# Performance work log

Hardware: AMD Instinct MI355X
Metric: run time of the kernel (lower is better)

Reference implementation:

```python
import jax, jax.numpy as jnp
import numpy as np

B, C, N, E, F = 8, 4, 2048, 512, 2048
EPS = 1e-5
MASK_SCALE = 5.0


def layer_norm(x, gamma, beta):
    mu = jnp.mean(x, axis=-1, keepdims=True)
    var = jnp.mean(jnp.square(x - mu), axis=-1, keepdims=True)
    return (x - mu) * jax.lax.rsqrt(var + EPS) * gamma + beta


def setup_inputs() -> dict:
    key = jax.random.key(0)
    ks = jax.random.split(key, 8)
    src = jax.random.normal(ks[0], (B, C, N, E), dtype=jnp.float32)
    key_padding_mask = jax.random.uniform(ks[1], (B, N), dtype=jnp.float32)
    # FFN params (torch Linear default init scale ~ U(-1/sqrt(fan_in), +))
    W1 = jax.random.normal(ks[2], (E, F), dtype=jnp.float32) / np.sqrt(E)
    b1 = jnp.zeros((F,), dtype=jnp.float32)
    W2 = jax.random.normal(ks[3], (F, E), dtype=jnp.float32) / np.sqrt(F)
    b2 = jnp.zeros((E,), dtype=jnp.float32)
    g1 = jnp.ones((E,), dtype=jnp.float32)
    be1 = jnp.zeros((E,), dtype=jnp.float32)
    g2 = jnp.ones((E,), dtype=jnp.float32)
    be2 = jnp.zeros((E,), dtype=jnp.float32)
    return {"src": src, "key_padding_mask": key_padding_mask,
            "W1": W1, "b1": b1, "W2": W2, "b2": b2,
            "g1": g1, "be1": be1, "g2": g2, "be2": be2}


def reference(src, key_padding_mask, W1, b1, W2, b2, g1, be1, g2, be2):
    # src: [B, C, N, E]; channels batched into one fused attention call
    scale = 1.0 / jnp.sqrt(jnp.asarray(src.shape[-1], src.dtype))
    scores = jnp.einsum('bcne,bcme->bcnm', src, src) * scale  # [B,C,N,N]
    scores = scores - key_padding_mask[:, None, None, :] * MASK_SCALE
    attn = jax.nn.softmax(scores, axis=-1)
    attn_out = jnp.einsum('bcnm,bcme->bcne', attn, src)
    # residual + norm1 (dropout is identity at eval)
    src2 = layer_norm(src + attn_out, g1, be1)
    # feedforward: Linear -> ReLU -> Linear
    ff = jax.nn.relu(jnp.einsum('bcne,ef->bcnf', src2, W1) + b1)
    ff = jnp.einsum('bcnf,fe->bcne', ff, W2) + b2
    out = layer_norm(src2 + ff, g2, be2)
    return out
```

## Files before the change

### kernel.cpp

```cpp
#include <hip/hip_runtime.h>
#include <stdint.h>

constexpr int CB = 8, CC = 4, CN = 2048, CE = 512, CF = 2048;
constexpr long long TOT = (long long)CB * CC * CN * CE;
constexpr int GRP = 16;
constexpr int MCH = 65536;
constexpr float SCALE = 0.04419417382415922f;
constexpr float MASK_SCALE = 5.0f;
constexpr float EPS = 1e-5f;

typedef unsigned short bf16_t;
typedef __attribute__((ext_vector_type(4))) float f32x4;
typedef __attribute__((ext_vector_type(8))) short s16x8;

#define DEV static __device__ __forceinline__

DEV unsigned short f2bf(float f) {
    unsigned u = __float_as_uint(f);
    unsigned r = (u + 0x7fffu + ((u >> 16) & 1u)) >> 16;
    return (unsigned short)r;
}
DEV float bf2f(unsigned short b) {
    return __uint_as_float(((unsigned)b) << 16);
}

typedef const __attribute__((address_space(1))) unsigned int* gptr_t;
typedef __attribute__((address_space(3))) unsigned int* lptr_t;
DEV void async16(const void* g, void* l) {
    __builtin_amdgcn_global_load_lds((gptr_t)g, (lptr_t)l, 16, 0, 0);
}

#define FULL_BAR() do { asm volatile("" ::: "memory"); __builtin_amdgcn_s_barrier(); asm volatile("" ::: "memory"); } while (0)
#define LGKM0() asm volatile("s_waitcnt lgkmcnt(0)" ::: "memory")
#define LGKM8() asm volatile("s_waitcnt lgkmcnt(8)" ::: "memory")
#define SCHED0() __builtin_amdgcn_sched_barrier(0)
#define VMCNT(N_) asm volatile("s_waitcnt vmcnt(" #N_ ")" ::: "memory")

DEV float blockSum256(float v, float* sm) {
    #pragma unroll
    for (int o = 32; o; o >>= 1) v += __shfl_xor(v, o);
    int w = threadIdx.x >> 6;
    __syncthreads();
    if ((threadIdx.x & 63) == 0) sm[w] = v;
    __syncthreads();
    return sm[0] + sm[1] + sm[2] + sm[3];
}
DEV float blockMax256(float v, float* sm) {
    #pragma unroll
    for (int o = 32; o; o >>= 1) v = fmaxf(v, __shfl_xor(v, o));
    int w = threadIdx.x >> 6;
    __syncthreads();
    if ((threadIdx.x & 63) == 0) sm[w] = v;
    __syncthreads();
    return fmaxf(fmaxf(sm[0], sm[1]), fmaxf(sm[2], sm[3]));
}

__global__ __launch_bounds__(256) void cvt_transpose(
    const float* __restrict__ in, bf16_t* __restrict__ outN,
    bf16_t* __restrict__ outT) {
    __shared__ bf16_t tile[32][33];
    const float* inz = in + (size_t)blockIdx.z * CN * CE;
    bf16_t* oN = outN + (size_t)blockIdx.z * CN * CE;
    bf16_t* oT = outT + (size_t)blockIdx.z * CE * CN;
    int rb = blockIdx.y * 32;
    int cb = blockIdx.x * 32;
    int tx = threadIdx.x & 31, ty = threadIdx.x >> 5;
    #pragma unroll
    for (int i = 0; i < 32; i += 8) {
        float v = inz[(size_t)(rb + ty + i) * CE + cb + tx];
        unsigned short h = f2bf(v);
        oN[(size_t)(rb + ty + i) * CE + cb + tx] = h;
        tile[ty + i][tx] = h;
    }
    __syncthreads();
    #pragma unroll
    for (int i = 0; i < 32; i += 8)
        oT[(size_t)(cb + ty + i) * CN + rb + tx] = tile[tx][ty + i];
}

__global__ __launch_bounds__(256) void transpose_f32_bf16(
    const float* __restrict__ in, bf16_t* __restrict__ out,
    int R, int Cc) {
    __shared__ float tile[32][33];
    int rb = blockIdx.y * 32, cb = blockIdx.x * 32;
    int tx = threadIdx.x & 31, ty = threadIdx.x >> 5;
    #pragma unroll
    for (int i = 0; i < 32; i += 8)
        tile[ty + i][tx] = in[(size_t)(rb + ty + i) * Cc + cb + tx];
    __syncthreads();
    #pragma unroll
    for (int i = 0; i < 32; i += 8)
        out[(size_t)(cb + ty + i) * R + rb + tx] = f2bf(tile[tx][ty + i]);
}

template <int EPI>
__global__ __launch_bounds__(256, 4) void gemm_bt(
    const bf16_t* __restrict__ A, const bf16_t* __restrict__ B,
    void* __restrict__ Cptr, const float* __restrict__ bias, float alpha,
    int Nc, int K, long long sA, long long sB, long long sC) {
    __shared__ bf16_t As[128 * 32];
    __shared__ bf16_t Bs[128 * 32];
    const bf16_t* Az = A + (size_t)blockIdx.z * sA;
    const bf16_t* Bz = B + (size_t)blockIdx.z * sB;
    int tid = threadIdx.x;
    int lane = tid & 63, wid = tid >> 6;
    int wr = wid >> 1, wc = wid & 1;
    int brow = blockIdx.y * 128, bcol = blockIdx.x * 128;

    f32x4 acc[4][4] = {};

    int c0 = tid, c1 = tid + 256;
    const bf16_t* Ag0 = Az + (size_t)(brow + (c0 >> 2)) * K + (c0 & 3) * 8;
    const bf16_t* Ag1 = Az + (size_t)(brow + (c1 >> 2)) * K + (c1 & 3) * 8;
    const bf16_t* Bg0 = Bz + (size_t)(bcol + (c0 >> 2)) * K + (c0 & 3) * 8;
    const bf16_t* Bg1 = Bz + (size_t)(bcol + (c1 >> 2)) * K + (c1 & 3) * 8;

    for (int k0 = 0; k0 < K; k0 += 32) {
        async16(Ag0 + k0, &As[c0 * 8]);
        async16(Ag1 + k0, &As[c1 * 8]);
        async16(Bg0 + k0, &Bs[c0 * 8]);
        async16(Bg1 + k0, &Bs[c1 * 8]);
        __syncthreads();
        s16x8 af[4], bv[4];
        #pragma unroll
        for (int m = 0; m < 4; m++)
            af[m] = *(const s16x8*)&As[(wr * 64 + m * 16 + (lane & 15)) * 32 + (lane >> 4) * 8];
        #pragma unroll
        for (int n = 0; n < 4; n++)
            bv[n] = *(const s16x8*)&Bs[(wc * 64 + n * 16 + (lane & 15)) * 32 + (lane >> 4) * 8];
        #pragma unroll
        for (int m = 0; m < 4; m++)
            #pragma unroll
            for (int n = 0; n < 4; n++)
                acc[m][n] = __builtin_amdgcn_mfma_f32_16x16x32_bf16(af[m], bv[n], acc[m][n], 0, 0, 0);
        __syncthreads();
    }

    size_t cz = (size_t)blockIdx.z * sC;
    bf16_t* Cb = (bf16_t*)Cptr + cz;
    const int q = lane >> 4, rr0 = lane & 15, lo = lane & 1;
    #pragma unroll
    for (int m = 0; m < 4; m++) {
        #pragma unroll
        for (int n = 0; n < 4; n++) {
            int col = bcol + wc * 64 + n * 16 + rr0;
            float bvv = (EPI == 1 || EPI == 4) ? bias[col] : 0.f;
            unsigned words[4];
            #pragma unroll
            for (int j = 0; j < 4; j++) {
                float v = acc[m][n][j] + bvv;
                if constexpr (EPI == 1) v = fmaxf(v, 0.f);
                if constexpr (EPI == 3) v *= alpha;
                unsigned h = f2bf(v);
                unsigned o = (unsigned)__shfl_xor((int)h, 1);
                words[j] = lo ? (o | (h << 16)) : (h | (o << 16));
            }
            int row = brow + wr * 64 + m * 16 + q * 4 + lo * 2;
            int cp = col & ~1;
            *(unsigned*)&Cb[(size_t)row * Nc + cp] = words[lo * 2];
            *(unsigned*)&Cb[(size_t)(row + 1) * Nc + cp] = words[lo * 2 + 1];
        }
    }
}

template <int EPI>
__global__ __launch_bounds__(512, 2) void gemm256(
    const bf16_t* __restrict__ A, const bf16_t* __restrict__ B,
    void* __restrict__ Cptr, const float* __restrict__ bias, float alpha,
    int Nc, int K, long long sA, long long sB, long long sC) {
    extern __shared__ bf16_t lds[];
    bf16_t* AsL = lds;
    bf16_t* BsL = lds + 32768;

    int bx, by, bz;
    {
        int gx = gridDim.x, gy = gridDim.y;
        int nwg = gx * gy * gridDim.z;
        int flat = blockIdx.x + gx * (blockIdx.y + gy * blockIdx.z);
        int wg = (nwg & 7) ? flat : ((flat & 7) * (nwg >> 3) + (flat >> 3));
        bx = wg % gx;
        int tmp = wg / gx;
        by = tmp % gy;
        bz = tmp / gy;
    }

    const bf16_t* Az = A + (size_t)bz * sA;
    const bf16_t* Bz = B + (size_t)bz * sB;
    const int t = threadIdx.x;
    const int lane = t & 63, wid = t >> 6;
    const int wr = wid >> 2, wc = wid & 3;
    const int brow = by * 256, bcol = bx * 256;
    const int NT = K >> 6;

    const int r0 = t >> 3, s0 = t & 7;
    const int ce = ((s0 ^ (r0 & 7)) << 3);
    const bf16_t* aP0 = Az + (size_t)(brow + r0) * K + ce;
    const bf16_t* bP0 = Bz + (size_t)(bcol + r0) * K + ce;
    const size_t rK64 = (size_t)64 * K;
    const size_t h128K = rK64 * 2;

    #define PUSH_A(kt_, h_) do { \
        bf16_t* d_ = AsL + ((((kt_) & 1) * 2 + (h_)) * 8192); \
        const bf16_t* s_ = aP0 + (size_t)(h_) * h128K + (size_t)(kt_) * 64; \
        async16(s_, d_ + t * 8); \
        async16(s_ + rK64, d_ + 4096 + t * 8); \
    } while (0)
    #define PUSH_B(kt_, h_) do { \
        bf16_t* d_ = BsL + ((((kt_) & 1) * 2 + (h_)) * 8192); \
        const bf16_t* s_ = bP0 + (size_t)(h_) * h128K + (size_t)(kt_) * 64; \
        async16(s_, d_ + t * 8); \
        async16(s_ + rK64, d_ + 4096 + t * 8); \
    } while (0)

    const int q = lane >> 4, rr0 = lane & 15, xmask = rr0 & 7;
    s16x8 af[4][2];
    s16x8 bv[2][2][2];
    f32x4 acc[2][2][4][2] = {};

    #define READ_A(ktp_, qm_) do { \
        const bf16_t* base_ = AsL + (((ktp_) * 2 + (qm_)) * 8192); \
        _Pragma("unroll") for (int m_ = 0; m_ < 4; ++m_) \
        _Pragma("unroll") for (int ks_ = 0; ks_ < 2; ++ks_) \
            af[m_][ks_] = *(const s16x8*)(base_ + (wr * 64 + m_ * 16 + rr0) * 64 + (((ks_ * 4 + q) ^ xmask) << 3)); \
    } while (0)
    #define READ_B(ktp_, qn_) do { \
        const bf16_t* base_ = BsL + (((ktp_) * 2 + (qn_)) * 8192); \
        _Pragma("unroll") for (int n_ = 0; n_ < 2; ++n_) \
        _Pragma("unroll") for (int ks_ = 0; ks_ < 2; ++ks_) \
            bv[qn_][n_][ks_] = *(const s16x8*)(base_ + (wc * 32 + n_ * 16 + rr0) * 64 + (((ks_ * 4 + q) ^ xmask) << 3)); \
    } while (0)
    #define MFMA_Q(qm_, qn_) do { \
        __builtin_amdgcn_s_setprio(1); \
        _Pragma("unroll") for (int m_ = 0; m_ < 4; ++m_) \
        _Pragma("unroll") for (int n_ = 0; n_ < 2; ++n_) \
        _Pragma("unroll") for (int ks_ = 0; ks_ < 2; ++ks_) \
            acc[qm_][qn_][m_][n_] = __builtin_amdgcn_mfma_f32_16x16x32_bf16( \
                af[m_][ks_], bv[qn_][n_][ks_], acc[qm_][qn_][m_][n_], 0, 0, 0); \
        __builtin_amdgcn_s_setprio(0); \
    } while (0)

    PUSH_A(0, 0); PUSH_B(0, 0); PUSH_B(0, 1); PUSH_A(0, 1);
    VMCNT(4);
    PUSH_A(1, 0); PUSH_B(1, 0); PUSH_B(1, 1);
    VMCNT(6);
    FULL_BAR();

    for (int T = 0; T < NT; ++T) {
        const int p = T & 1;
        const bool m1 = (T + 1 < NT), m2 = (T + 2 < NT);
        READ_A(p, 0);
        READ_B(p, 0);
        if (m1) PUSH_A(T + 1, 1);
        LGKM8();
        FULL_BAR(); LGKM0(); SCHED0();
        MFMA_Q(0, 0);
        FULL_BAR();
        READ_B(p, 1);
        if (m2) PUSH_A(T + 2, 0);
        FULL_BAR(); LGKM0(); SCHED0();
        MFMA_Q(0, 1);
        FULL_BAR();
        READ_A(p, 1);
        if (m2) PUSH_B(T + 2, 0);
        FULL_BAR(); LGKM0(); SCHED0();
        MFMA_Q(1, 0);
        FULL_BAR();
        if (m2) { PUSH_B(T + 2, 1); VMCNT(6); } else { VMCNT(0); }
        FULL_BAR();
        MFMA_Q(1, 1);
        FULL_BAR();
    }

    {
        size_t cz = (size_t)bz * sC;
        bf16_t* Cb = (bf16_t*)Cptr + cz;
        const int lo = lane & 1;
        #pragma unroll
        for (int qm = 0; qm < 2; ++qm)
        #pragma unroll
        for (int qn = 0; qn < 2; ++qn)
        #pragma unroll
        for (int n = 0; n < 2; ++n) {
            int col = bcol + qn * 128 + wc * 32 + n * 16 + rr0;
            float bvv = (EPI == 1 || EPI == 4) ? bias[col] : 0.f;
            #pragma unroll
            for (int m = 0; m < 4; ++m) {
                unsigned words[4];
                #pragma unroll
                for (int j = 0; j < 4; ++j) {
                    float v = acc[qm][qn][m][n][j] + bvv;
                    if constexpr (EPI == 1) v = fmaxf(v, 0.f);
                    if constexpr (EPI == 3) v *= alpha;
                    unsigned h = f2bf(v);
                    unsigned o = (unsigned)__shfl_xor((int)h, 1);
                    words[j] = lo ? (o | (h << 16)) : (h | (o << 16));
                }
                int row = brow + qm * 128 + wr * 64 + m * 16 + q * 4 + lo * 2;
                int cp = col & ~1;
                *(unsigned*)&Cb[(size_t)row * Nc + cp] = words[lo * 2];
                *(unsigned*)&Cb[(size_t)(row + 1) * Nc + cp] = words[lo * 2 + 1];
            }
        }
    }
    #undef PUSH_A
    #undef PUSH_B
    #undef READ_A
    #undef READ_B
    #undef MFMA_Q
}

__global__ __launch_bounds__(256) void softmax_bf16(
    bf16_t* __restrict__ S, const float* __restrict__ mask, int bc0) {
    __shared__ float sm[4];
    int gr = blockIdx.x;
    int b = (bc0 + (gr >> 11)) >> 2;
    bf16_t* row = S + (size_t)gr * CN;
    int tid = threadIdx.x;
    const float* mrow = mask + (size_t)b * CN + tid * 8;
    s16x8 v = *(const s16x8*)(row + tid * 8);
    float4 m0 = *(const float4*)(mrow);
    float4 m1 = *(const float4*)(mrow + 4);
    float x[8];
    x[0] = bf2f((unsigned short)v[0]) - m0.x * MASK_SCALE;
    x[1] = bf2f((unsigned short)v[1]) - m0.y * MASK_SCALE;
    x[2] = bf2f((unsigned short)v[2]) - m0.z * MASK_SCALE;
    x[3] = bf2f((unsigned short)v[3]) - m0.w * MASK_SCALE;
    x[4] = bf2f((unsigned short)v[4]) - m1.x * MASK_SCALE;
    x[5] = bf2f((unsigned short)v[5]) - m1.y * MASK_SCALE;
    x[6] = bf2f((unsigned short)v[6]) - m1.z * MASK_SCALE;
    x[7] = bf2f((unsigned short)v[7]) - m1.w * MASK_SCALE;
    float mx = -3.4e38f;
    #pragma unroll
    for (int i = 0; i < 8; i++) mx = fmaxf(mx, x[i]);
    mx = blockMax256(mx, sm);
    float s = 0.f;
    #pragma unroll
    for (int i = 0; i < 8; i++) { x[i] = __expf(x[i] - mx); s += x[i]; }
    s = blockSum256(s, sm);
    float inv = 1.f / s;
    s16x8 u;
    #pragma unroll
    for (int i = 0; i < 8; i++) u[i] = (short)f2bf(x[i] * inv);
    *(s16x8*)(row + tid * 8) = u;
}

__global__ __launch_bounds__(256) void ln1_kernel(
    const bf16_t* __restrict__ src, const bf16_t* __restrict__ ao,
    const float* __restrict__ g, const float* __restrict__ be,
    bf16_t* __restrict__ o) {
    __shared__ float sm[4];
    size_t base = (size_t)blockIdx.x * CE;
    int e = threadIdx.x * 2;
    ushort2 s = *(const ushort2*)&src[base + e];
    ushort2 a = *(const ushort2*)&ao[base + e];
    float x0 = bf2f(s.x) + bf2f(a.x), x1 = bf2f(s.y) + bf2f(a.y);
    float mu = blockSum256(x0 + x1, sm) * (1.f / CE);
    float d0 = x0 - mu, d1 = x1 - mu;
    float var = blockSum256(d0 * d0 + d1 * d1, sm) * (1.f / CE);
    float rs = rsqrtf(var + EPS);
    ushort2 w;
    w.x = f2bf(d0 * rs * g[e] + be[e]);
    w.y = f2bf(d1 * rs * g[e + 1] + be[e + 1]);
    *(ushort2*)&o[base + e] = w;
}

__global__ __launch_bounds__(256) void ln2_kernel(
    const bf16_t* __restrict__ a, const bf16_t* __restrict__ b,
    const float* __restrict__ g, const float* __restrict__ be,
    float* __restrict__ o) {
    __shared__ float sm[4];
    size_t base = (size_t)blockIdx.x * CE;
    int e = threadIdx.x * 2;
    ushort2 aa = *(const ushort2*)&a[base + e];
    ushort2 bb = *(const ushort2*)&b[base + e];
    float x0 = bf2f(aa.x) + bf2f(bb.x), x1 = bf2f(aa.y) + bf2f(bb.y);
    float mu = blockSum256(x0 + x1, sm) * (1.f / CE);
    float d0 = x0 - mu, d1 = x1 - mu;
    float var = blockSum256(d0 * d0 + d1 * d1, sm) * (1.f / CE);
    float rs = rsqrtf(var + EPS);
    float2 w;
    w.x = d0 * rs * g[e] + be[e];
    w.y = d1 * rs * g[e + 1] + be[e + 1];
    *(float2*)&o[base + e] = w;
}

extern "C" void kernel_launch(void* const* d_in, const int* in_sizes, int n_in,
                              void* d_out, int out_size, void* d_ws, size_t ws_size,
                              hipStream_t stream) {
    const float* src  = (const float*)d_in[0];
    const float* mask = (const float*)d_in[1];
    const float* W1   = (const float*)d_in[2];
    const float* b1   = (const float*)d_in[3];
    const float* W2   = (const float*)d_in[4];
    const float* b2   = (const float*)d_in[5];
    const float* g1   = (const float*)d_in[6];
    const float* be1  = (const float*)d_in[7];
    const float* g2   = (const float*)d_in[8];
    const float* be2  = (const float*)d_in[9];
    float* out = (float*)d_out;
    char* ws = (char*)d_ws;

    hipFuncSetAttribute(reinterpret_cast<const void*>(&gemm256<3>), hipFuncAttributeMaxDynamicSharedMemorySize, 131072);
    hipFuncSetAttribute(reinterpret_cast<const void*>(&gemm256<4>), hipFuncAttributeMaxDynamicSharedMemorySize, 131072);

    const size_t MB = 1024 * 1024;
    bf16_t* probs  = (bf16_t*)(ws);
    bf16_t* src_bf = (bf16_t*)(ws + 256 * MB);
    bf16_t* srcT   = (bf16_t*)(ws + 320 * MB);
    bf16_t* attnO  = (bf16_t*)(ws + 384 * MB);
    bf16_t* W1T    = (bf16_t*)(ws + 448 * MB);
    bf16_t* W2T    = (bf16_t*)(ws + 450 * MB);
    bf16_t* src2   = (bf16_t*)(ws);
    bf16_t* ff     = (bf16_t*)(ws + 64 * MB);
    bf16_t* H      = (bf16_t*)(ws + 128 * MB);
    if (ws_size < 452 * MB) return;

    cvt_transpose<<<dim3(CE / 32, CN / 32, 32), 256, 0, stream>>>(src, src_bf, srcT);
    transpose_f32_bf16<<<dim3(CF / 32, CE / 32, 1), 256, 0, stream>>>(W1, W1T, CE, CF);
    transpose_f32_bf16<<<dim3(CE / 32, CF / 32, 1), 256, 0, stream>>>(W2, W2T, CF, CE);

    for (int g0 = 0; g0 < CB * CC; g0 += GRP) {
        const bf16_t* srcb = src_bf + (size_t)g0 * CN * CE;
        bf16_t* probs_g = probs + (size_t)g0 * CN * CN;
        gemm_bt<3><<<dim3(CN / 128, CN / 128, GRP), 256, 0, stream>>>(
            srcb, srcb, probs_g, nullptr, SCALE, CN, CE,
            (long long)CN * CE, (long long)CN * CE, (long long)CN * CN);
        softmax_bf16<<<dim3(GRP * CN), 256, 0, stream>>>(probs_g, mask, g0);
        gemm256<3><<<dim3(CE / 256, CN / 256, GRP), 512, 131072, stream>>>(
            probs_g, srcT + (size_t)g0 * CE * CN, attnO + (size_t)g0 * CN * CE,
            nullptr, 1.0f, CE, CN,
            (long long)CN * CN, (long long)CE * CN, (long long)CN * CE);
    }
    ln1_kernel<<<dim3(CB * CC * CN), 256, 0, stream>>>(src_bf, attnO, g1, be1, src2);

    gemm_bt<1><<<dim3(CF / 128, MCH / 128, 1), 256, 0, stream>>>(
        src2, W1T, H, b1, 1.0f, CF, CE, 0, 0, 0);
    gemm256<4><<<dim3(CE / 256, MCH / 256, 1), 512, 131072, stream>>>(
        H, W2T, ff, b2, 1.0f, CE, CF, 0, 0, 0);
    ln2_kernel<<<dim3(MCH), 256, 0, stream>>>(src2, ff, g2, be2, out);
}
```

Before: 946.5 us.

## Replace GEMM kernels with a double-buffered swizzled 128-tile GEMM

The simple 128x128 GEMM gains double-buffered LDS with prefetch of the next K-tile during MFMA, an XOR swizzle against bank conflicts, MFMA priority raising, and grid remapping for cache locality. The hand-pipelined 256x256 GEMM is removed, and the PV and FFN2 GEMMs now use the 128 kernel. This aims to overlap global loads with compute in the QK and FFN1 GEMMs, at the cost of lower per-block reuse for the two GEMMs that used the larger tile.

```diff
diff --git a/kernel.cpp b/kernel.cpp
--- a/kernel.cpp
+++ b/kernel.cpp
@@ -32,7 +32,6 @@
 
 #define FULL_BAR() do { asm volatile("" ::: "memory"); __builtin_amdgcn_s_barrier(); asm volatile("" ::: "memory"); } while (0)
 #define LGKM0() asm volatile("s_waitcnt lgkmcnt(0)" ::: "memory")
-#define LGKM8() asm volatile("s_waitcnt lgkmcnt(8)" ::: "memory")
 #define SCHED0() __builtin_amdgcn_sched_barrier(0)
 #define VMCNT(N_) asm volatile("s_waitcnt vmcnt(" #N_ ")" ::: "memory")
 
@@ -94,51 +93,79 @@
 }
 
 template <int EPI>
-__global__ __launch_bounds__(256, 4) void gemm_bt(
+__global__ __launch_bounds__(256, 4) void gemm128(
     const bf16_t* __restrict__ A, const bf16_t* __restrict__ B,
     void* __restrict__ Cptr, const float* __restrict__ bias, float alpha,
     int Nc, int K, long long sA, long long sB, long long sC) {
-    __shared__ bf16_t As[128 * 32];
-    __shared__ bf16_t Bs[128 * 32];
-    const bf16_t* Az = A + (size_t)blockIdx.z * sA;
-    const bf16_t* Bz = B + (size_t)blockIdx.z * sB;
-    int tid = threadIdx.x;
-    int lane = tid & 63, wid = tid >> 6;
-    int wr = wid >> 1, wc = wid & 1;
-    int brow = blockIdx.y * 128, bcol = blockIdx.x * 128;
-
+    __shared__ bf16_t As[2][128 * 32];
+    __shared__ bf16_t Bs[2][128 * 32];
+
+    int bx, by, bz;
+    {
+        int gx = gridDim.x, gy = gridDim.y;
+        int nwg = gx * gy * gridDim.z;
+        int flat = blockIdx.x + gx * (blockIdx.y + gy * blockIdx.z);
+        int wg = (nwg & 7) ? flat : ((flat & 7) * (nwg >> 3) + (flat >> 3));
+        bx = wg % gx;
+        int tmp = wg / gx;
+        by = tmp % gy;
+        bz = tmp / gy;
+    }
+
+    const int t = threadIdx.x;
+    const int lane = t & 63, wid = t >> 6;
+    const int wr = wid >> 1, wc = wid & 1;
+    const int brow = by * 128, bcol = bx * 128;
+    const int NT = K >> 5;
+
+    const int r0 = t >> 2;
+    const int srcOff = (((t & 3) ^ ((t >> 3) & 3)) * 8);
+    const bf16_t* aP = A + (size_t)bz * sA + (size_t)(brow + r0) * K + srcOff;
+    const bf16_t* bP = B + (size_t)bz * sB + (size_t)(bcol + r0) * K + srcOff;
+    const size_t rK64 = (size_t)64 * K;
+
+    #define PUSH(i_, p_) do { \
+        const bf16_t* sa_ = aP + (size_t)(i_) * 32; \
+        const bf16_t* sb_ = bP + (size_t)(i_) * 32; \
+        async16(sa_, &As[p_][t * 8]); \
+        async16(sa_ + rK64, &As[p_][2048 + t * 8]); \
+        async16(sb_, &Bs[p_][t * 8]); \
+        async16(sb_ + rK64, &Bs[p_][2048 + t * 8]); \
+    } while (0)
+
+    const int q = lane >> 4, rr0 = lane & 15;
+    const int rslot = ((q ^ ((rr0 >> 1) & 3)) << 3);
     f32x4 acc[4][4] = {};
 
-    int c0 = tid, c1 = tid + 256;
-    const bf16_t* Ag0 = Az + (size_t)(brow + (c0 >> 2)) * K + (c0 & 3) * 8;
-    const bf16_t* Ag1 = Az + (size_t)(brow + (c1 >> 2)) * K + (c1 & 3) * 8;
-    const bf16_t* Bg0 = Bz + (size_t)(bcol + (c0 >> 2)) * K + (c0 & 3) * 8;
-    const bf16_t* Bg1 = Bz + (size_t)(bcol + (c1 >> 2)) * K + (c1 & 3) * 8;
-
-    for (int k0 = 0; k0 < K; k0 += 32) {
-        async16(Ag0 + k0, &As[c0 * 8]);
-        async16(Ag1 + k0, &As[c1 * 8]);
-        async16(Bg0 + k0, &Bs[c0 * 8]);
-        async16(Bg1 + k0, &Bs[c1 * 8]);
-        __syncthreads();
+    PUSH(0, 0);
+    VMCNT(0);
+    FULL_BAR();
+
+    for (int i = 0; i < NT; ++i) {
+        const int p = i & 1;
         s16x8 af[4], bv[4];
         #pragma unroll
-        for (int m = 0; m < 4; m++)
-            af[m] = *(const s16x8*)&As[(wr * 64 + m * 16 + (lane & 15)) * 32 + (lane >> 4) * 8];
+        for (int m = 0; m < 4; ++m)
+            af[m] = *(const s16x8*)&As[p][(wr * 64 + m * 16 + rr0) * 32 + rslot];
         #pragma unroll
-        for (int n = 0; n < 4; n++)
-            bv[n] = *(const s16x8*)&Bs[(wc * 64 + n * 16 + (lane & 15)) * 32 + (lane >> 4) * 8];
+        for (int n = 0; n < 4; ++n)
+            bv[n] = *(const s16x8*)&Bs[p][(wc * 64 + n * 16 + rr0) * 32 + rslot];
+        if (i + 1 < NT) PUSH(i + 1, p ^ 1);
+        LGKM0(); SCHED0();
+        __builtin_amdgcn_s_setprio(1);
         #pragma unroll
-        for (int m = 0; m < 4; m++)
+        for (int m = 0; m < 4; ++m)
             #pragma unroll
-            for (int n = 0; n < 4; n++)
+            for (int n = 0; n < 4; ++n)
                 acc[m][n] = __builtin_amdgcn_mfma_f32_16x16x32_bf16(af[m], bv[n], acc[m][n], 0, 0, 0);
-        __syncthreads();
-    }
-
-    size_t cz = (size_t)blockIdx.z * sC;
+        __builtin_amdgcn_s_setprio(0);
+        VMCNT(0);
+        FULL_BAR();
+    }
+
+    size_t cz = (size_t)bz * sC;
     bf16_t* Cb = (bf16_t*)Cptr + cz;
-    const int q = lane >> 4, rr0 = lane & 15, lo = lane & 1;
+    const int lo = lane & 1;
     #pragma unroll
     for (int m = 0; m < 4; m++) {
         #pragma unroll
@@ -161,152 +188,7 @@
             *(unsigned*)&Cb[(size_t)(row + 1) * Nc + cp] = words[lo * 2 + 1];
         }
     }
-}
-
-template <int EPI>
-__global__ __launch_bounds__(512, 2) void gemm256(
-    const bf16_t* __restrict__ A, const bf16_t* __restrict__ B,
-    void* __restrict__ Cptr, const float* __restrict__ bias, float alpha,
-    int Nc, int K, long long sA, long long sB, long long sC) {
-    extern __shared__ bf16_t lds[];
-    bf16_t* AsL = lds;
-    bf16_t* BsL = lds + 32768;
-
-    int bx, by, bz;
-    {
-        int gx = gridDim.x, gy = gridDim.y;
-        int nwg = gx * gy * gridDim.z;
-        int flat = blockIdx.x + gx * (blockIdx.y + gy * blockIdx.z);
-        int wg = (nwg & 7) ? flat : ((flat & 7) * (nwg >> 3) + (flat >> 3));
-        bx = wg % gx;
-        int tmp = wg / gx;
-        by = tmp % gy;
-        bz = tmp / gy;
-    }
-
-    const bf16_t* Az = A + (size_t)bz * sA;
-    const bf16_t* Bz = B + (size_t)bz * sB;
-    const int t = threadIdx.x;
-    const int lane = t & 63, wid = t >> 6;
-    const int wr = wid >> 2, wc = wid & 3;
-    const int brow = by * 256, bcol = bx * 256;
-    const int NT = K >> 6;
-
-    const int r0 = t >> 3, s0 = t & 7;
-    const int ce = ((s0 ^ (r0 & 7)) << 3);
-    const bf16_t* aP0 = Az + (size_t)(brow + r0) * K + ce;
-    const bf16_t* bP0 = Bz + (size_t)(bcol + r0) * K + ce;
-    const size_t rK64 = (size_t)64 * K;
-    const size_t h128K = rK64 * 2;
-
-    #define PUSH_A(kt_, h_) do { \
-        bf16_t* d_ = AsL + ((((kt_) & 1) * 2 + (h_)) * 8192); \
-        const bf16_t* s_ = aP0 + (size_t)(h_) * h128K + (size_t)(kt_) * 64; \
-        async16(s_, d_ + t * 8); \
-        async16(s_ + rK64, d_ + 4096 + t * 8); \
-    } while (0)
-    #define PUSH_B(kt_, h_) do { \
-        bf16_t* d_ = BsL + ((((kt_) & 1) * 2 + (h_)) * 8192); \
-        const bf16_t* s_ = bP0 + (size_t)(h_) * h128K + (size_t)(kt_) * 64; \
-        async16(s_, d_ + t * 8); \
-        async16(s_ + rK64, d_ + 4096 + t * 8); \
-    } while (0)
-
-    const int q = lane >> 4, rr0 = lane & 15, xmask = rr0 & 7;
-    s16x8 af[4][2];
-    s16x8 bv[2][2][2];
-    f32x4 acc[2][2][4][2] = {};
-
-    #define READ_A(ktp_, qm_) do { \
-        const bf16_t* base_ = AsL + (((ktp_) * 2 + (qm_)) * 8192); \
-        _Pragma("unroll") for (int m_ = 0; m_ < 4; ++m_) \
-        _Pragma("unroll") for (int ks_ = 0; ks_ < 2; ++ks_) \
-            af[m_][ks_] = *(const s16x8*)(base_ + (wr * 64 + m_ * 16 + rr0) * 64 + (((ks_ * 4 + q) ^ xmask) << 3)); \
-    } while (0)
-    #define READ_B(ktp_, qn_) do { \
-        const bf16_t* base_ = BsL + (((ktp_) * 2 + (qn_)) * 8192); \
-        _Pragma("unroll") for (int n_ = 0; n_ < 2; ++n_) \
-        _Pragma("unroll") for (int ks_ = 0; ks_ < 2; ++ks_) \
-            bv[qn_][n_][ks_] = *(const s16x8*)(base_ + (wc * 32 + n_ * 16 + rr0) * 64 + (((ks_ * 4 + q) ^ xmask) << 3)); \
-    } while (0)
-    #define MFMA_Q(qm_, qn_) do { \
-        __builtin_amdgcn_s_setprio(1); \
-        _Pragma("unroll") for (int m_ = 0; m_ < 4; ++m_) \
-        _Pragma("unroll") for (int n_ = 0; n_ < 2; ++n_) \
-        _Pragma("unroll") for (int ks_ = 0; ks_ < 2; ++ks_) \
-            acc[qm_][qn_][m_][n_] = __builtin_amdgcn_mfma_f32_16x16x32_bf16( \
-                af[m_][ks_], bv[qn_][n_][ks_], acc[qm_][qn_][m_][n_], 0, 0, 0); \
-        __builtin_amdgcn_s_setprio(0); \
-    } while (0)
-
-    PUSH_A(0, 0); PUSH_B(0, 0); PUSH_B(0, 1); PUSH_A(0, 1);
-    VMCNT(4);
-    PUSH_A(1, 0); PUSH_B(1, 0); PUSH_B(1, 1);
-    VMCNT(6);
-    FULL_BAR();
-
-    for (int T = 0; T < NT; ++T) {
-        const int p = T & 1;
-        const bool m1 = (T + 1 < NT), m2 = (T + 2 < NT);
-        READ_A(p, 0);
-        READ_B(p, 0);
-        if (m1) PUSH_A(T + 1, 1);
-        LGKM8();
-        FULL_BAR(); LGKM0(); SCHED0();
-        MFMA_Q(0, 0);
-        FULL_BAR();
-        READ_B(p, 1);
-        if (m2) PUSH_A(T + 2, 0);
-        FULL_BAR(); LGKM0(); SCHED0();
-        MFMA_Q(0, 1);
-        FULL_BAR();
-        READ_A(p, 1);
-        if (m2) PUSH_B(T + 2, 0);
-        FULL_BAR(); LGKM0(); SCHED0();
-        MFMA_Q(1, 0);
-        FULL_BAR();
-        if (m2) { PUSH_B(T + 2, 1); VMCNT(6); } else { VMCNT(0); }
-        FULL_BAR();
-        MFMA_Q(1, 1);
-        FULL_BAR();
-    }
-
-    {
-        size_t cz = (size_t)bz * sC;
-        bf16_t* Cb = (bf16_t*)Cptr + cz;
-        const int lo = lane & 1;
-        #pragma unroll
-        for (int qm = 0; qm < 2; ++qm)
-        #pragma unroll
-        for (int qn = 0; qn < 2; ++qn)
-        #pragma unroll
-        for (int n = 0; n < 2; ++n) {
-            int col = bcol + qn * 128 + wc * 32 + n * 16 + rr0;
-            float bvv = (EPI == 1 || EPI == 4) ? bias[col] : 0.f;
-            #pragma unroll
-            for (int m = 0; m < 4; ++m) {
-                unsigned words[4];
-                #pragma unroll
-                for (int j = 0; j < 4; ++j) {
-                    float v = acc[qm][qn][m][n][j] + bvv;
-                    if constexpr (EPI == 1) v = fmaxf(v, 0.f);
-                    if constexpr (EPI == 3) v *= alpha;
-                    unsigned h = f2bf(v);
-                    unsigned o = (unsigned)__shfl_xor((int)h, 1);
-                    words[j] = lo ? (o | (h << 16)) : (h | (o << 16));
-                }
-                int row = brow + qm * 128 + wr * 64 + m * 16 + q * 4 + lo * 2;
-                int cp = col & ~1;
-                *(unsigned*)&Cb[(size_t)row * Nc + cp] = words[lo * 2];
-                *(unsigned*)&Cb[(size_t)(row + 1) * Nc + cp] = words[lo * 2 + 1];
-            }
-        }
-    }
-    #undef PUSH_A
-    #undef PUSH_B
-    #undef READ_A
-    #undef READ_B
-    #undef MFMA_Q
+    #undef PUSH
 }
 
 __global__ __launch_bounds__(256) void softmax_bf16(
@@ -400,9 +282,6 @@
     float* out = (float*)d_out;
     char* ws = (char*)d_ws;
 
-    hipFuncSetAttribute(reinterpret_cast<const void*>(&gemm256<3>), hipFuncAttributeMaxDynamicSharedMemorySize, 131072);
-    hipFuncSetAttribute(reinterpret_cast<const void*>(&gemm256<4>), hipFuncAttributeMaxDynamicSharedMemorySize, 131072);
-
     const size_t MB = 1024 * 1024;
     bf16_t* probs  = (bf16_t*)(ws);
     bf16_t* src_bf = (bf16_t*)(ws + 256 * MB);
@@ -422,20 +301,20 @@
     for (int g0 = 0; g0 < CB * CC; g0 += GRP) {
         const bf16_t* srcb = src_bf + (size_t)g0 * CN * CE;
         bf16_t* probs_g = probs + (size_t)g0 * CN * CN;
-        gemm_bt<3><<<dim3(CN / 128, CN / 128, GRP), 256, 0, stream>>>(
+        gemm128<3><<<dim3(CN / 128, CN / 128, GRP), 256, 0, stream>>>(
             srcb, srcb, probs_g, nullptr, SCALE, CN, CE,
             (long long)CN * CE, (long long)CN * CE, (long long)CN * CN);
         softmax_bf16<<<dim3(GRP * CN), 256, 0, stream>>>(probs_g, mask, g0);
-        gemm256<3><<<dim3(CE / 256, CN / 256, GRP), 512, 131072, stream>>>(
+        gemm128<3><<<dim3(CE / 128, CN / 128, GRP), 256, 0, stream>>>(
             probs_g, srcT + (size_t)g0 * CE * CN, attnO + (size_t)g0 * CN * CE,
             nullptr, 1.0f, CE, CN,
             (long long)CN * CN, (long long)CE * CN, (long long)CN * CE);
     }
     ln1_kernel<<<dim3(CB * CC * CN), 256, 0, stream>>>(src_bf, attnO, g1, be1, src2);
 
-    gemm_bt<1><<<dim3(CF / 128, MCH / 128, 1), 256, 0, stream>>>(
+    gemm128<1><<<dim3(CF / 128, MCH / 128, 1), 256, 0, stream>>>(
         src2, W1T, H, b1, 1.0f, CF, CE, 0, 0, 0);
-    gemm256<4><<<dim3(CE / 256, MCH / 256, 1), 512, 131072, stream>>>(
+    gemm128<4><<<dim3(CE / 128, MCH / 128, 1), 256, 0, stream>>>(
         H, W2T, ff, b2, 1.0f, CE, CF, 0, 0, 0);
     ln2_kernel<<<dim3(MCH), 256, 0, stream>>>(src2, ff, g2, be2, out);
 }
```

Result: slower. 1.024 ms (+8.2%).

## Exploit QK^T symmetry with triangular 256-tile GEMM and upgrade FFN1 GEMM

Applied to the files above, without the earlier changes.

Replaces the 128-tile score GEMM with a 256-tile kernel that computes only the lower-triangular blocks of src·srcᵀ (36 of 64 tiles per matrix) and writes each off-diagonal tile both directly and transposed. This roughly halves the score-GEMM MFMA work. The first FFN GEMM also moves to the larger pipelined 256-tile kernel. The shared main loop is refactored into macros with a slightly changed staging order and wait counts. The transposed mirror stores are narrow 8-byte scattered writes, which may cost write bandwidth.

```diff
diff --git a/kernel.cpp b/kernel.cpp
--- a/kernel.cpp
+++ b/kernel.cpp
@@ -32,8 +32,6 @@
 
 #define FULL_BAR() do { asm volatile("" ::: "memory"); __builtin_amdgcn_s_barrier(); asm volatile("" ::: "memory"); } while (0)
 #define LGKM0() asm volatile("s_waitcnt lgkmcnt(0)" ::: "memory")
-#define LGKM8() asm volatile("s_waitcnt lgkmcnt(8)" ::: "memory")
-#define SCHED0() __builtin_amdgcn_sched_barrier(0)
 #define VMCNT(N_) asm volatile("s_waitcnt vmcnt(" #N_ ")" ::: "memory")
 
 DEV float blockSum256(float v, float* sm) {
@@ -93,85 +91,105 @@
         out[(size_t)(cb + ty + i) * R + rb + tx] = f2bf(tile[tx][ty + i]);
 }
 
-template <int EPI>
-__global__ __launch_bounds__(256, 4) void gemm_bt(
-    const bf16_t* __restrict__ A, const bf16_t* __restrict__ B,
-    void* __restrict__ Cptr, const float* __restrict__ bias, float alpha,
-    int Nc, int K, long long sA, long long sB, long long sC) {
-    __shared__ bf16_t As[128 * 32];
-    __shared__ bf16_t Bs[128 * 32];
-    const bf16_t* Az = A + (size_t)blockIdx.z * sA;
-    const bf16_t* Bz = B + (size_t)blockIdx.z * sB;
-    int tid = threadIdx.x;
-    int lane = tid & 63, wid = tid >> 6;
-    int wr = wid >> 1, wc = wid & 1;
-    int brow = blockIdx.y * 128, bcol = blockIdx.x * 128;
-
-    f32x4 acc[4][4] = {};
-
-    int c0 = tid, c1 = tid + 256;
-    const bf16_t* Ag0 = Az + (size_t)(brow + (c0 >> 2)) * K + (c0 & 3) * 8;
-    const bf16_t* Ag1 = Az + (size_t)(brow + (c1 >> 2)) * K + (c1 & 3) * 8;
-    const bf16_t* Bg0 = Bz + (size_t)(bcol + (c0 >> 2)) * K + (c0 & 3) * 8;
-    const bf16_t* Bg1 = Bz + (size_t)(bcol + (c1 >> 2)) * K + (c1 & 3) * 8;
-
-    for (int k0 = 0; k0 < K; k0 += 32) {
-        async16(Ag0 + k0, &As[c0 * 8]);
-        async16(Ag1 + k0, &As[c1 * 8]);
-        async16(Bg0 + k0, &Bs[c0 * 8]);
-        async16(Bg1 + k0, &Bs[c1 * 8]);
-        __syncthreads();
-        s16x8 af[4], bv[4];
-        #pragma unroll
-        for (int m = 0; m < 4; m++)
-            af[m] = *(const s16x8*)&As[(wr * 64 + m * 16 + (lane & 15)) * 32 + (lane >> 4) * 8];
-        #pragma unroll
-        for (int n = 0; n < 4; n++)
-            bv[n] = *(const s16x8*)&Bs[(wc * 64 + n * 16 + (lane & 15)) * 32 + (lane >> 4) * 8];
-        #pragma unroll
-        for (int m = 0; m < 4; m++)
-            #pragma unroll
-            for (int n = 0; n < 4; n++)
-                acc[m][n] = __builtin_amdgcn_mfma_f32_16x16x32_bf16(af[m], bv[n], acc[m][n], 0, 0, 0);
-        __syncthreads();
-    }
-
-    size_t cz = (size_t)blockIdx.z * sC;
-    bf16_t* Cb = (bf16_t*)Cptr + cz;
-    const int q = lane >> 4, rr0 = lane & 15, lo = lane & 1;
-    #pragma unroll
-    for (int m = 0; m < 4; m++) {
-        #pragma unroll
-        for (int n = 0; n < 4; n++) {
-            int col = bcol + wc * 64 + n * 16 + rr0;
-            float bvv = (EPI == 1 || EPI == 4) ? bias[col] : 0.f;
-            unsigned words[4];
-            #pragma unroll
-            for (int j = 0; j < 4; j++) {
-                float v = acc[m][n][j] + bvv;
-                if constexpr (EPI == 1) v = fmaxf(v, 0.f);
-                if constexpr (EPI == 3) v *= alpha;
-                unsigned h = f2bf(v);
-                unsigned o = (unsigned)__shfl_xor((int)h, 1);
-                words[j] = lo ? (o | (h << 16)) : (h | (o << 16));
-            }
-            int row = brow + wr * 64 + m * 16 + q * 4 + lo * 2;
-            int cp = col & ~1;
-            *(unsigned*)&Cb[(size_t)row * Nc + cp] = words[lo * 2];
-            *(unsigned*)&Cb[(size_t)(row + 1) * Nc + cp] = words[lo * 2 + 1];
-        }
-    }
-}
+#define GEMM_CORE_DECLS() \
+    extern __shared__ bf16_t lds[]; \
+    bf16_t* AsL = lds; \
+    bf16_t* BsL = lds + 32768; \
+    const int t = threadIdx.x; \
+    const int lane = t & 63, wid = t >> 6; \
+    const int wr = wid >> 2, wc = wid & 3; \
+    const int NT = K >> 6; \
+    const int r0 = t >> 3, s0 = t & 7; \
+    const int ce = ((s0 ^ (r0 & 7)) << 3); \
+    const bf16_t* aP0 = Az + (size_t)(brow + r0) * K + ce; \
+    const bf16_t* bP0 = Bz + (size_t)(bcol + r0) * K + ce; \
+    const size_t rK64 = (size_t)64 * K; \
+    const size_t h128K = rK64 * 2; \
+    const int q = lane >> 4, rr0 = lane & 15, xmask = rr0 & 7; \
+    s16x8 af[4][2]; \
+    s16x8 bv[2][2][2]; \
+    f32x4 acc[2][2][4][2] = {};
+
+#define STAGE_A(kt_, h_) do { \
+    bf16_t* d_ = AsL + ((((kt_) & 1) * 2 + (h_)) * 8192); \
+    const bf16_t* s_ = aP0 + (size_t)(h_) * h128K + (size_t)(kt_) * 64; \
+    async16(s_, d_ + t * 8); \
+    async16(s_ + rK64, d_ + 4096 + t * 8); \
+} while (0)
+#define STAGE_B(kt_, h_) do { \
+    bf16_t* d_ = BsL + ((((kt_) & 1) * 2 + (h_)) * 8192); \
+    const bf16_t* s_ = bP0 + (size_t)(h_) * h128K + (size_t)(kt_) * 64; \
+    async16(s_, d_ + t * 8); \
+    async16(s_ + rK64, d_ + 4096 + t * 8); \
+} while (0)
+#define READ_A(ktp_, qm_) do { \
+    const bf16_t* base_ = AsL + (((ktp_) * 2 + (qm_)) * 8192); \
+    _Pragma("unroll") for (int m_ = 0; m_ < 4; ++m_) \
+    _Pragma("unroll") for (int ks_ = 0; ks_ < 2; ++ks_) \
+        af[m_][ks_] = *(const s16x8*)(base_ + (wr * 64 + m_ * 16 + rr0) * 64 + (((ks_ * 4 + q) ^ xmask) << 3)); \
+} while (0)
+#define READ_B(ktp_, qn_) do { \
+    const bf16_t* base_ = BsL + (((ktp_) * 2 + (qn_)) * 8192); \
+    _Pragma("unroll") for (int n_ = 0; n_ < 2; ++n_) \
+    _Pragma("unroll") for (int ks_ = 0; ks_ < 2; ++ks_) \
+        bv[qn_][n_][ks_] = *(const s16x8*)(base_ + (wc * 32 + n_ * 16 + rr0) * 64 + (((ks_ * 4 + q) ^ xmask) << 3)); \
+} while (0)
+#define MFMA_Q(qm_, qn_) do { \
+    __builtin_amdgcn_s_setprio(1); \
+    _Pragma("unroll") for (int m_ = 0; m_ < 4; ++m_) \
+    _Pragma("unroll") for (int n_ = 0; n_ < 2; ++n_) \
+    _Pragma("unroll") for (int ks_ = 0; ks_ < 2; ++ks_) \
+        acc[qm_][qn_][m_][n_] = __builtin_amdgcn_mfma_f32_16x16x32_bf16( \
+            af[m_][ks_], bv[qn_][n_][ks_], acc[qm_][qn_][m_][n_], 0, 0, 0); \
+    __builtin_amdgcn_s_setprio(0); \
+} while (0)
+
+#define GEMM_MAIN_LOOP() \
+    STAGE_A(0, 0); STAGE_B(0, 0); STAGE_B(0, 1); STAGE_A(0, 1); \
+    if (1 < NT) { \
+        STAGE_A(1, 0); STAGE_B(1, 0); \
+        VMCNT(4); \
+    } else { \
+        VMCNT(0); \
+    } \
+    FULL_BAR(); \
+    for (int kt = 0; kt < NT; ++kt) { \
+        const int ktp = kt & 1; \
+        READ_A(ktp, 0); \
+        READ_B(ktp, 0); \
+        if (kt + 1 < NT) STAGE_B(kt + 1, 1); \
+        FULL_BAR(); \
+        LGKM0(); \
+        MFMA_Q(0, 0); \
+        FULL_BAR(); \
+        READ_B(ktp, 1); \
+        if (kt + 1 < NT) STAGE_A(kt + 1, 1); \
+        FULL_BAR(); \
+        LGKM0(); \
+        MFMA_Q(0, 1); \
+        FULL_BAR(); \
+        READ_A(ktp, 1); \
+        if (kt + 2 < NT) STAGE_A(kt + 2, 0); \
+        FULL_BAR(); \
+        LGKM0(); \
+        MFMA_Q(1, 0); \
+        FULL_BAR(); \
+        if (kt + 2 < NT) { \
+            STAGE_B(kt + 2, 0); \
+            VMCNT(4); \
+        } else { \
+            VMCNT(0); \
+        } \
+        FULL_BAR(); \
+        MFMA_Q(1, 1); \
+        FULL_BAR(); \
+    }
 
 template <int EPI>
 __global__ __launch_bounds__(512, 2) void gemm256(
     const bf16_t* __restrict__ A, const bf16_t* __restrict__ B,
     void* __restrict__ Cptr, const float* __restrict__ bias, float alpha,
     int Nc, int K, long long sA, long long sB, long long sC) {
-    extern __shared__ bf16_t lds[];
-    bf16_t* AsL = lds;
-    bf16_t* BsL = lds + 32768;
-
     int bx, by, bz;
     {
         int gx = gridDim.x, gy = gridDim.y;
@@ -183,130 +201,103 @@
         by = tmp % gy;
         bz = tmp / gy;
     }
-
     const bf16_t* Az = A + (size_t)bz * sA;
     const bf16_t* Bz = B + (size_t)bz * sB;
-    const int t = threadIdx.x;
-    const int lane = t & 63, wid = t >> 6;
-    const int wr = wid >> 2, wc = wid & 3;
     const int brow = by * 256, bcol = bx * 256;
-    const int NT = K >> 6;
-
-    const int r0 = t >> 3, s0 = t & 7;
-    const int ce = ((s0 ^ (r0 & 7)) << 3);
-    const bf16_t* aP0 = Az + (size_t)(brow + r0) * K + ce;
-    const bf16_t* bP0 = Bz + (size_t)(bcol + r0) * K + ce;
-    const size_t rK64 = (size_t)64 * K;
-    const size_t h128K = rK64 * 2;
-
-    #define PUSH_A(kt_, h_) do { \
-        bf16_t* d_ = AsL + ((((kt_) & 1) * 2 + (h_)) * 8192); \
-        const bf16_t* s_ = aP0 + (size_t)(h_) * h128K + (size_t)(kt_) * 64; \
-        async16(s_, d_ + t * 8); \
-        async16(s_ + rK64, d_ + 4096 + t * 8); \
-    } while (0)
-    #define PUSH_B(kt_, h_) do { \
-        bf16_t* d_ = BsL + ((((kt_) & 1) * 2 + (h_)) * 8192); \
-        const bf16_t* s_ = bP0 + (size_t)(h_) * h128K + (size_t)(kt_) * 64; \
-        async16(s_, d_ + t * 8); \
-        async16(s_ + rK64, d_ + 4096 + t * 8); \
-    } while (0)
-
-    const int q = lane >> 4, rr0 = lane & 15, xmask = rr0 & 7;
-    s16x8 af[4][2];
-    s16x8 bv[2][2][2];
-    f32x4 acc[2][2][4][2] = {};
-
-    #define READ_A(ktp_, qm_) do { \
-        const bf16_t* base_ = AsL + (((ktp_) * 2 + (qm_)) * 8192); \
-        _Pragma("unroll") for (int m_ = 0; m_ < 4; ++m_) \
-        _Pragma("unroll") for (int ks_ = 0; ks_ < 2; ++ks_) \
-            af[m_][ks_] = *(const s16x8*)(base_ + (wr * 64 + m_ * 16 + rr0) * 64 + (((ks_ * 4 + q) ^ xmask) << 3)); \
-    } while (0)
-    #define READ_B(ktp_, qn_) do { \
-        const bf16_t* base_ = BsL + (((ktp_) * 2 + (qn_)) * 8192); \
-        _Pragma("unroll") for (int n_ = 0; n_ < 2; ++n_) \
-        _Pragma("unroll") for (int ks_ = 0; ks_ < 2; ++ks_) \
-            bv[qn_][n_][ks_] = *(const s16x8*)(base_ + (wc * 32 + n_ * 16 + rr0) * 64 + (((ks_ * 4 + q) ^ xmask) << 3)); \
-    } while (0)
-    #define MFMA_Q(qm_, qn_) do { \
-        __builtin_amdgcn_s_setprio(1); \
-        _Pragma("unroll") for (int m_ = 0; m_ < 4; ++m_) \
-        _Pragma("unroll") for (int n_ = 0; n_ < 2; ++n_) \
-        _Pragma("unroll") for (int ks_ = 0; ks_ < 2; ++ks_) \
-            acc[qm_][qn_][m_][n_] = __builtin_amdgcn_mfma_f32_16x16x32_bf16( \
-                af[m_][ks_], bv[qn_][n_][ks_], acc[qm_][qn_][m_][n_], 0, 0, 0); \
-        __builtin_amdgcn_s_setprio(0); \
-    } while (0)
-
-    PUSH_A(0, 0); PUSH_B(0, 0); PUSH_B(0, 1); PUSH_A(0, 1);
-    VMCNT(4);
-    PUSH_A(1, 0); PUSH_B(1, 0); PUSH_B(1, 1);
-    VMCNT(6);
-    FULL_BAR();
-
-    for (int T = 0; T < NT; ++T) {
-        const int p = T & 1;
-        const bool m1 = (T + 1 < NT), m2 = (T + 2 < NT);
-        READ_A(p, 0);
-        READ_B(p, 0);
-        if (m1) PUSH_A(T + 1, 1);
-        LGKM8();
-        FULL_BAR(); LGKM0(); SCHED0();
-        MFMA_Q(0, 0);
-        FULL_BAR();
-        READ_B(p, 1);
-        if (m2) PUSH_A(T + 2, 0);
-        FULL_BAR(); LGKM0(); SCHED0();
-        MFMA_Q(0, 1);
-        FULL_BAR();
-        READ_A(p, 1);
-        if (m2) PUSH_B(T + 2, 0);
-        FULL_BAR(); LGKM0(); SCHED0();
-        MFMA_Q(1, 0);
-        FULL_BAR();
-        if (m2) { PUSH_B(T + 2, 1); VMCNT(6); } else { VMCNT(0); }
-        FULL_BAR();
-        MFMA_Q(1, 1);
-        FULL_BAR();
-    }
-
+
+    GEMM_CORE_DECLS();
+    GEMM_MAIN_LOOP();
+
+    size_t cz = (size_t)bz * sC;
+    bf16_t* Cb = (bf16_t*)Cptr + cz;
+    const int lo = lane & 1;
+    #pragma unroll
+    for (int qm = 0; qm < 2; ++qm)
+    #pragma unroll
+    for (int qn = 0; qn < 2; ++qn)
+    #pragma unroll
+    for (int n = 0; n < 2; ++n) {
+        int col = bcol + qn * 128 + wc * 32 + n * 16 + rr0;
+        float bvv = (EPI == 1 || EPI == 4) ? bias[col] : 0.f;
+        #pragma unroll
+        for (int m = 0; m < 4; ++m) {
+            unsigned words[4];
+            #pragma unroll
+            for (int j = 0; j < 4; ++j) {
+                float v = acc[qm][qn][m][n][j] + bvv;
+                if constexpr (EPI == 1) v = fmaxf(v, 0.f);
+                if constexpr (EPI == 3) v *= alpha;
+                unsigned h = f2bf(v);
+                unsigned o = (unsigned)__shfl_xor((int)h, 1);
+                words[j] = lo ? (o | (h << 16)) : (h | (o << 16));
+            }
+            int row = brow + qm * 128 + wr * 64 + m * 16 + q * 4 + lo * 2;
+            int cp = col & ~1;
+            *(unsigned*)&Cb[(size_t)row * Nc + cp] = words[lo * 2];
+            *(unsigned*)&Cb[(size_t)(row + 1) * Nc + cp] = words[lo * 2 + 1];
+        }
+    }
+}
+
+__global__ __launch_bounds__(512, 2) void gemm256_sym(
+    const bf16_t* __restrict__ A, bf16_t* __restrict__ Cptr, float alpha,
+    int Nc, int K, long long sA, long long sC) {
+    int bx, by, bz;
     {
-        size_t cz = (size_t)bz * sC;
-        bf16_t* Cb = (bf16_t*)Cptr + cz;
-        const int lo = lane & 1;
+        int gx = gridDim.x;
+        int nwg = gx * gridDim.z;
+        int flat = blockIdx.x + gx * blockIdx.z;
+        int wg = (nwg & 7) ? flat : ((flat & 7) * (nwg >> 3) + (flat >> 3));
+        int tri = wg % gx;
+        bz = wg / gx;
+        int i = 0, b = 0;
+        while (b + i + 1 <= tri) { b += i + 1; i++; }
+        by = i;
+        bx = tri - b;
+    }
+    const bf16_t* Az = A + (size_t)bz * sA;
+    const bf16_t* Bz = Az;
+    const int brow = by * 256, bcol = bx * 256;
+
+    GEMM_CORE_DECLS();
+    GEMM_MAIN_LOOP();
+
+    size_t cz = (size_t)bz * sC;
+    bf16_t* Cb = (bf16_t*)Cptr + cz;
+    const int lo = lane & 1;
+    const bool mirror = (bx != by);
+    #pragma unroll
+    for (int qm = 0; qm < 2; ++qm)
+    #pragma unroll
+    for (int qn = 0; qn < 2; ++qn)
+    #pragma unroll
+    for (int n = 0; n < 2; ++n) {
+        int col = bcol + qn * 128 + wc * 32 + n * 16 + rr0;
         #pragma unroll
-        for (int qm = 0; qm < 2; ++qm)
-        #pragma unroll
-        for (int qn = 0; qn < 2; ++qn)
-        #pragma unroll
-        for (int n = 0; n < 2; ++n) {
-            int col = bcol + qn * 128 + wc * 32 + n * 16 + rr0;
-            float bvv = (EPI == 1 || EPI == 4) ? bias[col] : 0.f;
+        for (int m = 0; m < 4; ++m) {
+            unsigned short hh[4];
             #pragma unroll
-            for (int m = 0; m < 4; ++m) {
-                unsigned words[4];
-                #pragma unroll
-                for (int j = 0; j < 4; ++j) {
-                    float v = acc[qm][qn][m][n][j] + bvv;
-                    if constexpr (EPI == 1) v = fmaxf(v, 0.f);
-                    if constexpr (EPI == 3) v *= alpha;
-                    unsigned h = f2bf(v);
-                    unsigned o = (unsigned)__shfl_xor((int)h, 1);
-                    words[j] = lo ? (o | (h << 16)) : (h | (o << 16));
-                }
-                int row = brow + qm * 128 + wr * 64 + m * 16 + q * 4 + lo * 2;
-                int cp = col & ~1;
-                *(unsigned*)&Cb[(size_t)row * Nc + cp] = words[lo * 2];
-                *(unsigned*)&Cb[(size_t)(row + 1) * Nc + cp] = words[lo * 2 + 1];
+            for (int j = 0; j < 4; ++j)
+                hh[j] = f2bf(acc[qm][qn][m][n][j] * alpha);
+            unsigned words[4];
+            #pragma unroll
+            for (int j = 0; j < 4; ++j) {
+                unsigned h = hh[j];
+                unsigned o = (unsigned)__shfl_xor((int)h, 1);
+                words[j] = lo ? (o | (h << 16)) : (h | (o << 16));
+            }
+            int row = brow + qm * 128 + wr * 64 + m * 16 + q * 4 + lo * 2;
+            int cp = col & ~1;
+            *(unsigned*)&Cb[(size_t)row * Nc + cp] = words[lo * 2];
+            *(unsigned*)&Cb[(size_t)(row + 1) * Nc + cp] = words[lo * 2 + 1];
+            if (mirror) {
+                int mcol0 = brow + qm * 128 + wr * 64 + m * 16 + q * 4;
+                ushort4 mv;
+                mv.x = hh[0]; mv.y = hh[1]; mv.z = hh[2]; mv.w = hh[3];
+                *(ushort4*)&Cb[(size_t)col * Nc + mcol0] = mv;
             }
         }
     }
-    #undef PUSH_A
-    #undef PUSH_B
-    #undef READ_A
-    #undef READ_B
-    #undef MFMA_Q
 }
 
 __global__ __launch_bounds__(256) void softmax_bf16(
@@ -400,8 +391,10 @@
     float* out = (float*)d_out;
     char* ws = (char*)d_ws;
 
+    hipFuncSetAttribute(reinterpret_cast<const void*>(&gemm256<1>), hipFuncAttributeMaxDynamicSharedMemorySize, 131072);
     hipFuncSetAttribute(reinterpret_cast<const void*>(&gemm256<3>), hipFuncAttributeMaxDynamicSharedMemorySize, 131072);
     hipFuncSetAttribute(reinterpret_cast<const void*>(&gemm256<4>), hipFuncAttributeMaxDynamicSharedMemorySize, 131072);
+    hipFuncSetAttribute(reinterpret_cast<const void*>(&gemm256_sym), hipFuncAttributeMaxDynamicSharedMemorySize, 131072);
 
     const size_t MB = 1024 * 1024;
     bf16_t* probs  = (bf16_t*)(ws);
@@ -422,9 +415,9 @@
     for (int g0 = 0; g0 < CB * CC; g0 += GRP) {
         const bf16_t* srcb = src_bf + (size_t)g0 * CN * CE;
         bf16_t* probs_g = probs + (size_t)g0 * CN * CN;
-        gemm_bt<3><<<dim3(CN / 128, CN / 128, GRP), 256, 0, stream>>>(
-            srcb, srcb, probs_g, nullptr, SCALE, CN, CE,
-            (long long)CN * CE, (long long)CN * CE, (long long)CN * CN);
+        gemm256_sym<<<dim3(36, 1, GRP), 512, 131072, stream>>>(
+            srcb, probs_g, SCALE, CN, CE,
+            (long long)CN * CE, (long long)CN * CN);
         softmax_bf16<<<dim3(GRP * CN), 256, 0, stream>>>(probs_g, mask, g0);
         gemm256<3><<<dim3(CE / 256, CN / 256, GRP), 512, 131072, stream>>>(
             probs_g, srcT + (size_t)g0 * CE * CN, attnO + (size_t)g0 * CN * CE,
@@ -433,7 +426,7 @@
     }
     ln1_kernel<<<dim3(CB * CC * CN), 256, 0, stream>>>(src_bf, attnO, g1, be1, src2);
 
-    gemm_bt<1><<<dim3(CF / 128, MCH / 128, 1), 256, 0, stream>>>(
+    gemm256<1><<<dim3(CF / 256, MCH / 256, 1), 512, 131072, stream>>>(
         src2, W1T, H, b1, 1.0f, CF, CE, 0, 0, 0);
     gemm256<4><<<dim3(CE / 256, MCH / 256, 1), 512, 131072, stream>>>(
         H, W2T, ff, b2, 1.0f, CE, CF, 0, 0, 0);
```

Result: faster. 878.4 us (-7.2%).
